# Kernel optimization log

Hardware: AMD Instinct MI355X
Metric: run time of the kernel (lower is better)

The kernel has to match this reference:

```python
import jax, jax.numpy as jnp
import numpy as np

EPS = 1e-5
SCALE = 0.25
H = 16  # num_heads

def _bn(x, gamma, beta):
    # training-mode BatchNorm1d over (batch, length) per channel; x: [M, C, N]
    mean = jnp.mean(x, axis=(0, 2), keepdims=True)
    var = jnp.var(x, axis=(0, 2), keepdims=True)
    return gamma[None, :, None] * (x - mean) * jax.lax.rsqrt(var + EPS) + beta[None, :, None]

def _spike(x, vth):
    # fresh MyNode within one forward: mem = 0/tau + x, spike if >= vth
    return (x >= vth).astype(x.dtype)

def setup_inputs() -> dict:
    key = jax.random.key(0)
    ks = jax.random.split(key, 8)
    T, B, C, N = 4, 1, 256, 1024
    x = jax.random.normal(ks[0], (T, B, C, N), dtype=jnp.float32)
    y = jax.random.normal(ks[1], (T, B, C, N), dtype=jnp.float32)
    def w(k):
        return jax.random.normal(k, (C, C), dtype=jnp.float32) * (1.0 / np.sqrt(C))
    return {
        "x": x, "y": y,
        "Wq": w(ks[2]), "gq": jnp.ones((C,), jnp.float32), "bq": jnp.zeros((C,), jnp.float32),
        "Wk": w(ks[3]), "gk": jnp.ones((C,), jnp.float32), "bk": jnp.zeros((C,), jnp.float32),
        "Wv": w(ks[4]), "gv": jnp.ones((C,), jnp.float32), "bv": jnp.zeros((C,), jnp.float32),
        "Wp": w(ks[5]), "gp": jnp.ones((C,), jnp.float32), "bp": jnp.zeros((C,), jnp.float32),
    }

def reference(x, y, Wq, gq, bq, Wk, gk, bk, Wv, gv, bv, Wp, gp, bp):
    T, B, C, N = x.shape
    D = C // H
    xf = x.reshape(T * B, C, N)
    yf = y.reshape(T * B, C, N)

    def branch(inp, W, g, b, vth):
        h = jnp.einsum('oc,mcn->mon', W, inp)      # conv1x1
        h = _bn(h, g, b)
        s = _spike(h, vth)                          # LIF spike (fresh state)
        # [T,B,C,N] -> split channels into heads -> [T,B,H,N,D]
        return s.reshape(T, B, H, D, N).transpose(0, 1, 2, 4, 3)

    q = branch(xf, Wq, gq, bq, 1.0)
    k = branch(yf, Wk, gk, bk, 1.0)
    v = branch(yf, Wv, gv, bv, 1.0)

    attn = jnp.einsum('tbhnd,tbhmd->tbhnm', q, k)   # [T,B,H,N,N]
    out = jnp.einsum('tbhnm,tbhmd->tbhnd', attn, v) * SCALE

    # [T,B,H,N,D] -> [T,B,C,N]
    out = out.transpose(0, 1, 2, 4, 3).reshape(T, B, C, N)
    out = _spike(out.reshape(T * B, C, N), 0.5)      # attn_lif, v_threshold=0.5
    out = jnp.einsum('oc,mcn->mon', Wp, out)         # proj conv1x1
    out = _spike(_bn(out, gp, bp), 1.0)              # proj_bn + proj_lif
    return out.reshape(T, B, C, N)
```

## Files before the change

kernel.cpp:

```cpp
#include <hip/hip_runtime.h>
#include <cstdint>
#include <cstddef>

static constexpr int C = 256;
static constexpr int N = 1024;
static constexpr int M = 4;
static constexpr size_t PLANE = (size_t)M * C * N;

typedef double d4 __attribute__((ext_vector_type(4)));

__device__ inline void probe_d_layout(int lane, int rowv[4], int colv[4])
{
    const double am = (lane < 16) ? (double)lane : 0.0;
    const double a1 = (lane < 16) ? 1.0 : 0.0;
    const double bn = (lane < 16) ? (double)(lane & 15) : 0.0;
    d4 z = (d4){0.0, 0.0, 0.0, 0.0};
    d4 dr = __builtin_amdgcn_mfma_f64_16x16x4f64(am, a1, z, 0, 0, 0);
    d4 dc = __builtin_amdgcn_mfma_f64_16x16x4f64(a1, bn, z, 0, 0, 0);
    #pragma unroll
    for (int r = 0; r < 4; ++r) {
        rowv[r] = (int)dr[r];
        colv[r] = (int)dc[r];
    }
}

static constexpr int ASTR = 36;
static constexpr int BSTR = 72;

__global__ __launch_bounds__(256) void gemm_qkv_mfma(
    const float* __restrict__ x, const float* __restrict__ y,
    const float* __restrict__ Wq, const float* __restrict__ Wk,
    const float* __restrict__ Wv, double* __restrict__ hbase)
{
    const int bz = blockIdx.z;
    const int br = bz >> 2;
    const int m  = bz & 3;
    const float* __restrict__ W = (br == 0) ? Wq : (br == 1) ? Wk : Wv;
    const float* __restrict__ X = ((br == 0) ? x : y) + (size_t)m * C * N;
    double* __restrict__ H = hbase + (size_t)br * PLANE + (size_t)m * C * N;

    const int n0 = blockIdx.x * 64;
    const int o0 = blockIdx.y * 64;
    const int tid  = threadIdx.x;
    const int lane = tid & 63;
    const int w    = tid >> 6;
    const int ow   = (w & 1) * 32;
    const int nw   = (w >> 1) * 32;
    const int lm   = lane & 15;
    const int lk   = lane >> 4;

    int rowv[4], colv[4];
    probe_d_layout(lane, rowv, colv);

    __shared__ __align__(16) float As[2][64 * ASTR];
    __shared__ __align__(16) float Bs[2][32 * BSTR];

    d4 acc[2][2];
    #pragma unroll
    for (int i = 0; i < 2; ++i)
        #pragma unroll
        for (int j = 0; j < 2; ++j)
            acc[i][j] = (d4){0.0, 0.0, 0.0, 0.0};

    const int rA = tid >> 2;
    const int cA = (tid & 3) * 8;
    const int rB = tid >> 3;
    const int cB = (tid & 7) * 8;

    float4 a0r, a1r, b0r, b1r;
    a0r = *(const float4*)(W + (size_t)(o0 + rA) * C + 0 + cA);
    a1r = *(const float4*)(W + (size_t)(o0 + rA) * C + 0 + cA + 4);
    b0r = *(const float4*)(X + (size_t)(0 + rB) * N + n0 + cB);
    b1r = *(const float4*)(X + (size_t)(0 + rB) * N + n0 + cB + 4);

    int buf = 0;
    for (int ch = 0; ch < 8; ++ch) {
        *(float4*)(&As[buf][rA * ASTR + cA])     = a0r;
        *(float4*)(&As[buf][rA * ASTR + cA + 4]) = a1r;
        *(float4*)(&Bs[buf][rB * BSTR + cB])     = b0r;
        *(float4*)(&Bs[buf][rB * BSTR + cB + 4]) = b1r;
        __syncthreads();
        if (ch < 7) {
            const int c0 = (ch + 1) * 32;
            a0r = *(const float4*)(W + (size_t)(o0 + rA) * C + c0 + cA);
            a1r = *(const float4*)(W + (size_t)(o0 + rA) * C + c0 + cA + 4);
            b0r = *(const float4*)(X + (size_t)(c0 + rB) * N + n0 + cB);
            b1r = *(const float4*)(X + (size_t)(c0 + rB) * N + n0 + cB + 4);
        }
        const float* __restrict__ Ab = As[buf];
        const float* __restrict__ Bb = Bs[buf];
        #pragma unroll
        for (int ks = 0; ks < 8; ++ks) {
            const int kk = ks * 4 + lk;
            double a0 = (double)Ab[(ow + lm) * ASTR + kk];
            double a1 = (double)Ab[(ow + 16 + lm) * ASTR + kk];
            double b0 = (double)Bb[kk * BSTR + nw + lm];
            double b1 = (double)Bb[kk * BSTR + nw + 16 + lm];
            acc[0][0] = __builtin_amdgcn_mfma_f64_16x16x4f64(a0, b0, acc[0][0], 0, 0, 0);
            acc[0][1] = __builtin_amdgcn_mfma_f64_16x16x4f64(a0, b1, acc[0][1], 0, 0, 0);
            acc[1][0] = __builtin_amdgcn_mfma_f64_16x16x4f64(a1, b0, acc[1][0], 0, 0, 0);
            acc[1][1] = __builtin_amdgcn_mfma_f64_16x16x4f64(a1, b1, acc[1][1], 0, 0, 0);
        }
        buf ^= 1;
    }

    #pragma unroll
    for (int ot = 0; ot < 2; ++ot)
        #pragma unroll
        for (int nt = 0; nt < 2; ++nt)
            #pragma unroll
            for (int r = 0; r < 4; ++r)
                H[(size_t)(o0 + ow + ot * 16 + rowv[r]) * N + (n0 + nw + nt * 16 + colv[r])] =
                    acc[ot][nt][r];
}

__global__ __launch_bounds__(256) void gemm_p_mfma(
    const float* __restrict__ Wp, const unsigned char* __restrict__ s2,
    double* __restrict__ hp)
{
    const int m = blockIdx.z;
    const unsigned char* __restrict__ X = s2 + (size_t)m * C * N;
    double* __restrict__ H = hp + (size_t)m * C * N;

    const int n0 = blockIdx.x * 64;
    const int o0 = blockIdx.y * 32;
    const int tid  = threadIdx.x;
    const int lane = tid & 63;
    const int w    = tid >> 6;
    const int ow   = (w & 1) * 16;
    const int nw   = (w >> 1) * 32;
    const int lm   = lane & 15;
    const int lk   = lane >> 4;

    int rowv[4], colv[4];
    probe_d_layout(lane, rowv, colv);

    __shared__ __align__(16) float As[2][32 * ASTR];
    __shared__ __align__(16) float Bs[2][32 * BSTR];

    d4 acc[2];
    acc[0] = (d4){0.0, 0.0, 0.0, 0.0};
    acc[1] = (d4){0.0, 0.0, 0.0, 0.0};

    const int rA = tid >> 3;
    const int cA = (tid & 7) * 4;
    const int rB = tid >> 3;
    const int cB = (tid & 7) * 8;

    float4 ar;
    uint2 bw;
    ar = *(const float4*)(Wp + (size_t)(o0 + rA) * C + 0 + cA);
    bw = *(const uint2*)(X + (size_t)(0 + rB) * N + n0 + cB);

    int buf = 0;
    for (int ch = 0; ch < 8; ++ch) {
        *(float4*)(&As[buf][rA * ASTR + cA]) = ar;
        float* bs = &Bs[buf][rB * BSTR + cB];
        bs[0] = (float)(bw.x & 0xFF);
        bs[1] = (float)((bw.x >> 8) & 0xFF);
        bs[2] = (float)((bw.x >> 16) & 0xFF);
        bs[3] = (float)((bw.x >> 24) & 0xFF);
        bs[4] = (float)(bw.y & 0xFF);
        bs[5] = (float)((bw.y >> 8) & 0xFF);
        bs[6] = (float)((bw.y >> 16) & 0xFF);
        bs[7] = (float)((bw.y >> 24) & 0xFF);
        __syncthreads();
        if (ch < 7) {
            const int c0 = (ch + 1) * 32;
            ar = *(const float4*)(Wp + (size_t)(o0 + rA) * C + c0 + cA);
            bw = *(const uint2*)(X + (size_t)(c0 + rB) * N + n0 + cB);
        }
        const float* __restrict__ Ab = As[buf];
        const float* __restrict__ Bb = Bs[buf];
        #pragma unroll
        for (int ks = 0; ks < 8; ++ks) {
            const int kk = ks * 4 + lk;
            double a0 = (double)Ab[(ow + lm) * ASTR + kk];
            double b0 = (double)Bb[kk * BSTR + nw + lm];
            double b1 = (double)Bb[kk * BSTR + nw + 16 + lm];
            acc[0] = __builtin_amdgcn_mfma_f64_16x16x4f64(a0, b0, acc[0], 0, 0, 0);
            acc[1] = __builtin_amdgcn_mfma_f64_16x16x4f64(a0, b1, acc[1], 0, 0, 0);
        }
        buf ^= 1;
    }

    #pragma unroll
    for (int nt = 0; nt < 2; ++nt)
        #pragma unroll
        for (int r = 0; r < 4; ++r)
            H[(size_t)(o0 + ow + rowv[r]) * N + (n0 + nw + nt * 16 + colv[r])] =
                acc[nt][r];
}

__global__ __launch_bounds__(256) void bnspike_qkv(
    const double* __restrict__ hbase,
    const float* __restrict__ gq, const float* __restrict__ bq,
    const float* __restrict__ gk, const float* __restrict__ bk,
    const float* __restrict__ gv, const float* __restrict__ bv,
    unsigned char* __restrict__ sbase)
{
    const int o  = blockIdx.x;
    const int br = blockIdx.y;
    const double* __restrict__ h = hbase + (size_t)br * PLANE + (size_t)o * N;
    const int tid = threadIdx.x;

    double2 v[8];
    double s = 0.0, ss = 0.0;
    #pragma unroll
    for (int j = 0; j < 8; ++j) {
        int idx = j * 512 + tid * 2;
        int mm = idx >> 10, nn = idx & 1023;
        v[j] = *(const double2*)(h + (size_t)mm * C * N + nn);
        s  += v[j].x + v[j].y;
        ss += v[j].x * v[j].x + v[j].y * v[j].y;
    }
    #pragma unroll
    for (int off = 32; off > 0; off >>= 1) {
        s  += __shfl_down(s, off, 64);
        ss += __shfl_down(ss, off, 64);
    }
    __shared__ double rs[4], rss[4], sstat[2];
    const int lane = tid & 63, wv_ = tid >> 6;
    if (lane == 0) { rs[wv_] = s; rss[wv_] = ss; }
    __syncthreads();
    if (tid == 0) {
        double S  = rs[0] + rs[1] + rs[2] + rs[3];
        double SS = rss[0] + rss[1] + rss[2] + rss[3];
        double mean = S / 4096.0;
        double var  = SS / 4096.0 - mean * mean;
        sstat[0] = mean;
        sstat[1] = 1.0 / sqrt(var + 1e-5);
    }
    __syncthreads();
    const double mean = sstat[0], inv = sstat[1];
    const float* g = (br == 0) ? gq : (br == 1) ? gk : gv;
    const float* b = (br == 0) ? bq : (br == 1) ? bk : bv;
    const double gc = (double)g[o], bc = (double)b[o];
    unsigned char* out = sbase + (size_t)br * PLANE + (size_t)o * N;
    #pragma unroll
    for (int j = 0; j < 8; ++j) {
        int idx = j * 512 + tid * 2;
        int mm = idx >> 10, nn = idx & 1023;
        double t0 = gc * (v[j].x - mean) * inv + bc;
        double t1 = gc * (v[j].y - mean) * inv + bc;
        unsigned short pk = (unsigned short)((t0 >= 1.0) ? 1u : 0u) |
                            (unsigned short)(((t1 >= 1.0) ? 1u : 0u) << 8);
        *(unsigned short*)(out + (size_t)mm * C * N + nn) = pk;
    }
}

__global__ __launch_bounds__(256) void attn_kernel(
    const unsigned char* __restrict__ qb, const unsigned char* __restrict__ kb,
    const unsigned char* __restrict__ vb, unsigned char* __restrict__ s2)
{
    const int nc = blockIdx.x;
    const int hh = blockIdx.y;
    const int t  = blockIdx.z;
    const int tid = threadIdx.x;

    __shared__ unsigned int kw[16][257];
    __shared__ unsigned int vw[16][257];
    __shared__ int kt[256];

    #pragma unroll
    for (int j = 0; j < 4; ++j) {
        int idx = j * 256 + tid;
        int r = idx >> 6, q4 = idx & 63;
        size_t goff = ((size_t)(t * C + hh * 16 + r)) * N + (size_t)q4 * 16;
        uint4 kk = *(const uint4*)(kb + goff);
        uint4 vv = *(const uint4*)(vb + goff);
        kw[r][q4 * 4 + 0] = kk.x; kw[r][q4 * 4 + 1] = kk.y;
        kw[r][q4 * 4 + 2] = kk.z; kw[r][q4 * 4 + 3] = kk.w;
        vw[r][q4 * 4 + 0] = vv.x; vw[r][q4 * 4 + 1] = vv.y;
        vw[r][q4 * 4 + 2] = vv.z; vw[r][q4 * 4 + 3] = vv.w;
    }
    __syncthreads();

    const int d = tid >> 4, dp = tid & 15;
    int sum = 0;
    #pragma unroll 8
    for (int wd = 0; wd < 256; ++wd)
        sum += __popc(kw[d][wd] & vw[dp][wd]);
    kt[tid] = sum;
    __syncthreads();

    const int n = nc * 256 + tid;
    int sums[16];
    #pragma unroll
    for (int i = 0; i < 16; ++i) sums[i] = 0;
    #pragma unroll
    for (int d2 = 0; d2 < 16; ++d2) {
        int qv = (int)qb[((size_t)(t * C + hh * 16 + d2)) * N + n];
        #pragma unroll
        for (int dp2 = 0; dp2 < 16; ++dp2)
            sums[dp2] += qv * kt[d2 * 16 + dp2];
    }
    #pragma unroll
    for (int dp2 = 0; dp2 < 16; ++dp2)
        s2[((size_t)(t * C + hh * 16 + dp2)) * N + n] = (sums[dp2] >= 2) ? 1 : 0;
}

__global__ __launch_bounds__(256) void bnspike_p(
    const double* __restrict__ hp,
    const float* __restrict__ gp, const float* __restrict__ bp,
    float* __restrict__ outp)
{
    const int o = blockIdx.x;
    const double* __restrict__ h = hp + (size_t)o * N;
    const int tid = threadIdx.x;

    double2 v[8];
    double s = 0.0, ss = 0.0;
    #pragma unroll
    for (int j = 0; j < 8; ++j) {
        int idx = j * 512 + tid * 2;
        int mm = idx >> 10, nn = idx & 1023;
        v[j] = *(const double2*)(h + (size_t)mm * C * N + nn);
        s  += v[j].x + v[j].y;
        ss += v[j].x * v[j].x + v[j].y * v[j].y;
    }
    #pragma unroll
    for (int off = 32; off > 0; off >>= 1) {
        s  += __shfl_down(s, off, 64);
        ss += __shfl_down(ss, off, 64);
    }
    __shared__ double rs[4], rss[4], sstat[2];
    const int lane = tid & 63, wv_ = tid >> 6;
    if (lane == 0) { rs[wv_] = s; rss[wv_] = ss; }
    __syncthreads();
    if (tid == 0) {
        double S  = rs[0] + rs[1] + rs[2] + rs[3];
        double SS = rss[0] + rss[1] + rss[2] + rss[3];
        double mean = S / 4096.0;
        double var  = SS / 4096.0 - mean * mean;
        sstat[0] = mean;
        sstat[1] = 1.0 / sqrt(var + 1e-5);
    }
    __syncthreads();
    const double mean = sstat[0], inv = sstat[1];
    const double gc = (double)gp[o], bc = (double)bp[o];
    float* out = outp + (size_t)o * N;
    #pragma unroll
    for (int j = 0; j < 8; ++j) {
        int idx = j * 512 + tid * 2;
        int mm = idx >> 10, nn = idx & 1023;
        float2 r;
        r.x = (gc * (v[j].x - mean) * inv + bc >= 1.0) ? 1.0f : 0.0f;
        r.y = (gc * (v[j].y - mean) * inv + bc >= 1.0) ? 1.0f : 0.0f;
        *(float2*)(out + (size_t)mm * C * N + nn) = r;
    }
}

extern "C" void kernel_launch(void* const* d_in, const int* in_sizes, int n_in,
                              void* d_out, int out_size, void* d_ws, size_t ws_size,
                              hipStream_t stream)
{
    const float* x  = (const float*)d_in[0];
    const float* y  = (const float*)d_in[1];
    const float* Wq = (const float*)d_in[2];
    const float* gq = (const float*)d_in[3];
    const float* bq = (const float*)d_in[4];
    const float* Wk = (const float*)d_in[5];
    const float* gk = (const float*)d_in[6];
    const float* bk = (const float*)d_in[7];
    const float* Wv = (const float*)d_in[8];
    const float* gv = (const float*)d_in[9];
    const float* bv = (const float*)d_in[10];
    const float* Wp = (const float*)d_in[11];
    const float* gp = (const float*)d_in[12];
    const float* bp = (const float*)d_in[13];
    float* out = (float*)d_out;

    char* ws = (char*)d_ws;
    double* hq = (double*)ws;
    double* hp = hq;
    unsigned char* qb  = (unsigned char*)(ws + 3 * PLANE * sizeof(double));
    unsigned char* kb2 = qb + PLANE;
    unsigned char* vb2 = qb + 2 * PLANE;
    unsigned char* s2b = qb + 3 * PLANE;

    gemm_qkv_mfma<<<dim3(16, 4, 12), 256, 0, stream>>>(x, y, Wq, Wk, Wv, hq);
    bnspike_qkv<<<dim3(256, 3), 256, 0, stream>>>(hq, gq, bq, gk, bk, gv, bv, qb);
    attn_kernel<<<dim3(4, 16, 4), 256, 0, stream>>>(qb, kb2, vb2, s2b);
    gemm_p_mfma<<<dim3(16, 8, 4), 256, 0, stream>>>(Wp, s2b, hp);
    bnspike_p<<<dim3(256), 256, 0, stream>>>(hp, gp, bp, out);
}
```

Baseline: 148.5 us.

## Replace FP64 MFMA GEMMs with three-way split FP16 MFMA emulation

```diff
diff --git a/kernel.cpp b/kernel.cpp
--- a/kernel.cpp
+++ b/kernel.cpp
@@ -1,229 +1,239 @@
 #include <hip/hip_runtime.h>
 #include <cstdint>
 #include <cstddef>
+#include <cmath>
 
 static constexpr int C = 256;
 static constexpr int N = 1024;
 static constexpr int M = 4;
 static constexpr size_t PLANE = (size_t)M * C * N;
 
-typedef double d4 __attribute__((ext_vector_type(4)));
-
-__device__ inline void probe_d_layout(int lane, int rowv[4], int colv[4])
-{
-    const double am = (lane < 16) ? (double)lane : 0.0;
-    const double a1 = (lane < 16) ? 1.0 : 0.0;
-    const double bn = (lane < 16) ? (double)(lane & 15) : 0.0;
-    d4 z = (d4){0.0, 0.0, 0.0, 0.0};
-    d4 dr = __builtin_amdgcn_mfma_f64_16x16x4f64(am, a1, z, 0, 0, 0);
-    d4 dc = __builtin_amdgcn_mfma_f64_16x16x4f64(a1, bn, z, 0, 0, 0);
-    #pragma unroll
-    for (int r = 0; r < 4; ++r) {
-        rowv[r] = (int)dr[r];
-        colv[r] = (int)dc[r];
-    }
-}
-
-static constexpr int ASTR = 36;
-static constexpr int BSTR = 72;
-
-__global__ __launch_bounds__(256) void gemm_qkv_mfma(
+typedef unsigned short u16;
+typedef u16      u16x8 __attribute__((ext_vector_type(8)));
+typedef u16      u16x4 __attribute__((ext_vector_type(4)));
+typedef _Float16 f16x8 __attribute__((ext_vector_type(8)));
+typedef float    f32x4 __attribute__((ext_vector_type(4)));
+
+static constexpr int FSTR = 40;
+static constexpr size_t LVX = (size_t)8 * 1024 * 256;
+static constexpr size_t LVW = (size_t)4 * 256 * 256;
+
+__device__ __forceinline__ void split3(float v, u16 &h0, u16 &h1, u16 &h2)
+{
+    union { _Float16 f; u16 u; } cv;
+    float a0 = (fabsf(v) >= 6.103515625e-05f) ? v : 0.0f;
+    cv.f = (_Float16)a0;                 h0 = cv.u;
+    float f0 = (float)cv.f;
+    float r1 = v - f0;
+    cv.f = (_Float16)(r1 * 4096.0f);     h1 = cv.u;
+    float f1 = (float)cv.f * 2.44140625e-4f;
+    float r2 = r1 - f1;
+    cv.f = (_Float16)(r2 * 16777216.0f); h2 = cv.u;
+}
+
+__device__ __forceinline__ void probe16(int lane, int rowv[4], int colv[4])
+{
+    f16x8 ar, one, bn;
+    #pragma unroll
+    for (int i = 0; i < 8; ++i){ ar[i]=(_Float16)0.f; one[i]=(_Float16)0.f; bn[i]=(_Float16)0.f; }
+    if (lane < 16){
+        ar[0]  = (_Float16)(float)lane;
+        one[0] = (_Float16)1.0f;
+        bn[0]  = (_Float16)(float)lane;
+    }
+    f32x4 z = (f32x4){0.f,0.f,0.f,0.f};
+    f32x4 dr = __builtin_amdgcn_mfma_f32_16x16x32_f16(ar,  one, z, 0, 0, 0);
+    f32x4 dc = __builtin_amdgcn_mfma_f32_16x16x32_f16(one, bn,  z, 0, 0, 0);
+    #pragma unroll
+    for (int r = 0; r < 4; ++r){ rowv[r] = (int)dr[r]; colv[r] = (int)dc[r]; }
+}
+
+__global__ __launch_bounds__(256) void split_pre(
     const float* __restrict__ x, const float* __restrict__ y,
     const float* __restrict__ Wq, const float* __restrict__ Wk,
-    const float* __restrict__ Wv, double* __restrict__ hbase)
-{
-    const int bz = blockIdx.z;
-    const int br = bz >> 2;
-    const int m  = bz & 3;
-    const float* __restrict__ W = (br == 0) ? Wq : (br == 1) ? Wk : Wv;
-    const float* __restrict__ X = ((br == 0) ? x : y) + (size_t)m * C * N;
-    double* __restrict__ H = hbase + (size_t)br * PLANE + (size_t)m * C * N;
-
-    const int n0 = blockIdx.x * 64;
-    const int o0 = blockIdx.y * 64;
-    const int tid  = threadIdx.x;
-    const int lane = tid & 63;
-    const int w    = tid >> 6;
-    const int ow   = (w & 1) * 32;
-    const int nw   = (w >> 1) * 32;
-    const int lm   = lane & 15;
-    const int lk   = lane >> 4;
+    const float* __restrict__ Wv, const float* __restrict__ Wp,
+    u16* __restrict__ xyT, u16* __restrict__ wsp)
+{
+    const int z = blockIdx.z, tid = threadIdx.x;
+    if (z < 8){
+        const float* __restrict__ src = (z < 4) ? (x + (size_t)z * C * N)
+                                                : (y + (size_t)(z - 4) * C * N);
+        const int n0 = blockIdx.x * 64, c0 = blockIdx.y * 64;
+        __shared__ float Ls[64][65];
+        const int cr = tid >> 2, q = tid & 3;
+        #pragma unroll
+        for (int j = 0; j < 4; ++j){
+            float4 vv = *(const float4*)(src + (size_t)(c0 + cr) * N + n0 + q * 16 + j * 4);
+            *(float4*)&Ls[cr][q * 16 + j * 4] = vv;
+        }
+        __syncthreads();
+        const int nr = tid >> 2, cq = tid & 3;
+        u16 h0[16], h1[16], h2[16];
+        #pragma unroll
+        for (int e = 0; e < 16; ++e)
+            split3(Ls[cq * 16 + e][nr], h0[e], h1[e], h2[e]);
+        const size_t base = (size_t)z * (1024 * 256) + (size_t)(n0 + nr) * C + c0 + cq * 16;
+        u16x8 t0, t1;
+        #pragma unroll
+        for (int i = 0; i < 8; ++i){ t0[i] = h0[i]; t1[i] = h0[8 + i]; }
+        *(u16x8*)(xyT + base) = t0;            *(u16x8*)(xyT + base + 8) = t1;
+        #pragma unroll
+        for (int i = 0; i < 8; ++i){ t0[i] = h1[i]; t1[i] = h1[8 + i]; }
+        *(u16x8*)(xyT + LVX + base) = t0;      *(u16x8*)(xyT + LVX + base + 8) = t1;
+        #pragma unroll
+        for (int i = 0; i < 8; ++i){ t0[i] = h2[i]; t1[i] = h2[8 + i]; }
+        *(u16x8*)(xyT + 2 * LVX + base) = t0;  *(u16x8*)(xyT + 2 * LVX + base + 8) = t1;
+    } else {
+        const float* __restrict__ Wm = (z == 8) ? Wq : (z == 9) ? Wk : (z == 10) ? Wv : Wp;
+        const int idx = ((blockIdx.y * 16 + blockIdx.x) * 256 + tid) * 4;
+        float4 vv = *(const float4*)(Wm + idx);
+        const size_t base = (size_t)(z - 8) * 65536 + idx;
+        u16x4 o0_, o1_, o2_;
+        u16 a, b, c2;
+        split3(vv.x, a, b, c2); o0_[0]=a; o1_[0]=b; o2_[0]=c2;
+        split3(vv.y, a, b, c2); o0_[1]=a; o1_[1]=b; o2_[1]=c2;
+        split3(vv.z, a, b, c2); o0_[2]=a; o1_[2]=b; o2_[2]=c2;
+        split3(vv.w, a, b, c2); o0_[3]=a; o1_[3]=b; o2_[3]=c2;
+        *(u16x4*)(wsp + base) = o0_;
+        *(u16x4*)(wsp + LVW + base) = o1_;
+        *(u16x4*)(wsp + 2 * LVW + base) = o2_;
+    }
+}
+
+__global__ __launch_bounds__(256, 2) void gemm_qkv_f16(
+    const u16* __restrict__ xyT, const u16* __restrict__ wsp,
+    float* __restrict__ hbase)
+{
+    const int bz = blockIdx.z, br = bz >> 2, m = bz & 3;
+    const int plane = (br == 0) ? m : 4 + m;
+    const u16* __restrict__ Xl = xyT + (size_t)plane * 1024 * 256;
+    const u16* __restrict__ Wl = wsp + (size_t)br * 65536;
+    float* __restrict__ H = hbase + (size_t)br * PLANE + (size_t)m * C * N;
+
+    const int n0 = blockIdx.x * 64, o0 = blockIdx.y * 64;
+    const int tid = threadIdx.x, lane = tid & 63, w = tid >> 6;
+    const int ow = (w & 1) * 32, nw = (w >> 1) * 32, lm = lane & 15, lk = lane >> 4;
 
     int rowv[4], colv[4];
-    probe_d_layout(lane, rowv, colv);
-
-    __shared__ __align__(16) float As[2][64 * ASTR];
-    __shared__ __align__(16) float Bs[2][32 * BSTR];
-
-    d4 acc[2][2];
+    probe16(lane, rowv, colv);
+
+    __shared__ __align__(16) u16 As[2][3][64 * FSTR];
+    __shared__ __align__(16) u16 Bs[2][3][64 * FSTR];
+
+    f32x4 ah[2][2], am2[2][2], al[2][2];
+    double hs[2][2][4];
     #pragma unroll
     for (int i = 0; i < 2; ++i)
         #pragma unroll
-        for (int j = 0; j < 2; ++j)
-            acc[i][j] = (d4){0.0, 0.0, 0.0, 0.0};
-
-    const int rA = tid >> 2;
-    const int cA = (tid & 3) * 8;
-    const int rB = tid >> 3;
-    const int cB = (tid & 7) * 8;
-
-    float4 a0r, a1r, b0r, b1r;
-    a0r = *(const float4*)(W + (size_t)(o0 + rA) * C + 0 + cA);
-    a1r = *(const float4*)(W + (size_t)(o0 + rA) * C + 0 + cA + 4);
-    b0r = *(const float4*)(X + (size_t)(0 + rB) * N + n0 + cB);
-    b1r = *(const float4*)(X + (size_t)(0 + rB) * N + n0 + cB + 4);
+        for (int j = 0; j < 2; ++j){
+            ah[i][j] = (f32x4){0.f,0.f,0.f,0.f};
+            am2[i][j] = (f32x4){0.f,0.f,0.f,0.f};
+            al[i][j] = (f32x4){0.f,0.f,0.f,0.f};
+            #pragma unroll
+            for (int r = 0; r < 4; ++r) hs[i][j][r] = 0.0;
+        }
+
+    const int rA = tid >> 2, c8 = (tid & 3) * 8;
+    u16x8 aR[3], bR[3];
+    #pragma unroll
+    for (int lv = 0; lv < 3; ++lv){
+        aR[lv] = *(const u16x8*)(Wl + (size_t)lv * LVW + (size_t)(o0 + rA) * C + c8);
+        bR[lv] = *(const u16x8*)(Xl + (size_t)lv * LVX + (size_t)(n0 + rA) * C + c8);
+    }
 
     int buf = 0;
-    for (int ch = 0; ch < 8; ++ch) {
-        *(float4*)(&As[buf][rA * ASTR + cA])     = a0r;
-        *(float4*)(&As[buf][rA * ASTR + cA + 4]) = a1r;
-        *(float4*)(&Bs[buf][rB * BSTR + cB])     = b0r;
-        *(float4*)(&Bs[buf][rB * BSTR + cB + 4]) = b1r;
+    for (int ch = 0; ch < 8; ++ch){
+        #pragma unroll
+        for (int lv = 0; lv < 3; ++lv){
+            *(u16x8*)&As[buf][lv][rA * FSTR + c8] = aR[lv];
+            *(u16x8*)&Bs[buf][lv][rA * FSTR + c8] = bR[lv];
+        }
         __syncthreads();
-        if (ch < 7) {
-            const int c0 = (ch + 1) * 32;
-            a0r = *(const float4*)(W + (size_t)(o0 + rA) * C + c0 + cA);
-            a1r = *(const float4*)(W + (size_t)(o0 + rA) * C + c0 + cA + 4);
-            b0r = *(const float4*)(X + (size_t)(c0 + rB) * N + n0 + cB);
-            b1r = *(const float4*)(X + (size_t)(c0 + rB) * N + n0 + cB + 4);
-        }
-        const float* __restrict__ Ab = As[buf];
-        const float* __restrict__ Bb = Bs[buf];
-        #pragma unroll
-        for (int ks = 0; ks < 8; ++ks) {
-            const int kk = ks * 4 + lk;
-            double a0 = (double)Ab[(ow + lm) * ASTR + kk];
-            double a1 = (double)Ab[(ow + 16 + lm) * ASTR + kk];
-            double b0 = (double)Bb[kk * BSTR + nw + lm];
-            double b1 = (double)Bb[kk * BSTR + nw + 16 + lm];
-            acc[0][0] = __builtin_amdgcn_mfma_f64_16x16x4f64(a0, b0, acc[0][0], 0, 0, 0);
-            acc[0][1] = __builtin_amdgcn_mfma_f64_16x16x4f64(a0, b1, acc[0][1], 0, 0, 0);
-            acc[1][0] = __builtin_amdgcn_mfma_f64_16x16x4f64(a1, b0, acc[1][0], 0, 0, 0);
-            acc[1][1] = __builtin_amdgcn_mfma_f64_16x16x4f64(a1, b1, acc[1][1], 0, 0, 0);
+        if (ch < 7){
+            const int cc = (ch + 1) * 32;
+            #pragma unroll
+            for (int lv = 0; lv < 3; ++lv){
+                aR[lv] = *(const u16x8*)(Wl + (size_t)lv * LVW + (size_t)(o0 + rA) * C + cc + c8);
+                bR[lv] = *(const u16x8*)(Xl + (size_t)lv * LVX + (size_t)(n0 + rA) * C + cc + c8);
+            }
+        }
+        f16x8 af[2][3], bf[2][3];
+        #pragma unroll
+        for (int ot = 0; ot < 2; ++ot)
+            #pragma unroll
+            for (int lv = 0; lv < 3; ++lv)
+                af[ot][lv] = *(const f16x8*)&As[buf][lv][(ow + ot * 16 + lm) * FSTR + lk * 8];
+        #pragma unroll
+        for (int nt = 0; nt < 2; ++nt)
+            #pragma unroll
+            for (int lv = 0; lv < 3; ++lv)
+                bf[nt][lv] = *(const f16x8*)&Bs[buf][lv][(nw + nt * 16 + lm) * FSTR + lk * 8];
+        #pragma unroll
+        for (int ot = 0; ot < 2; ++ot)
+            #pragma unroll
+            for (int nt = 0; nt < 2; ++nt){
+                ah[ot][nt]  = __builtin_amdgcn_mfma_f32_16x16x32_f16(af[ot][0], bf[nt][0], ah[ot][nt], 0, 0, 0);
+                am2[ot][nt] = __builtin_amdgcn_mfma_f32_16x16x32_f16(af[ot][0], bf[nt][1], am2[ot][nt], 0, 0, 0);
+                am2[ot][nt] = __builtin_amdgcn_mfma_f32_16x16x32_f16(af[ot][1], bf[nt][0], am2[ot][nt], 0, 0, 0);
+                al[ot][nt]  = __builtin_amdgcn_mfma_f32_16x16x32_f16(af[ot][1], bf[nt][1], al[ot][nt], 0, 0, 0);
+                al[ot][nt]  = __builtin_amdgcn_mfma_f32_16x16x32_f16(af[ot][0], bf[nt][2], al[ot][nt], 0, 0, 0);
+                al[ot][nt]  = __builtin_amdgcn_mfma_f32_16x16x32_f16(af[ot][2], bf[nt][0], al[ot][nt], 0, 0, 0);
+            }
+        if (ch & 1){
+            #pragma unroll
+            for (int ot = 0; ot < 2; ++ot)
+                #pragma unroll
+                for (int nt = 0; nt < 2; ++nt){
+                    #pragma unroll
+                    for (int r = 0; r < 4; ++r) hs[ot][nt][r] += (double)ah[ot][nt][r];
+                    ah[ot][nt] = (f32x4){0.f,0.f,0.f,0.f};
+                }
         }
         buf ^= 1;
     }
 
+    const double S12 = 1.0 / 4096.0, S24 = 1.0 / 16777216.0;
     #pragma unroll
     for (int ot = 0; ot < 2; ++ot)
         #pragma unroll
         for (int nt = 0; nt < 2; ++nt)
             #pragma unroll
-            for (int r = 0; r < 4; ++r)
-                H[(size_t)(o0 + ow + ot * 16 + rowv[r]) * N + (n0 + nw + nt * 16 + colv[r])] =
-                    acc[ot][nt][r];
-}
-
-__global__ __launch_bounds__(256) void gemm_p_mfma(
-    const float* __restrict__ Wp, const unsigned char* __restrict__ s2,
-    double* __restrict__ hp)
-{
-    const int m = blockIdx.z;
-    const unsigned char* __restrict__ X = s2 + (size_t)m * C * N;
-    double* __restrict__ H = hp + (size_t)m * C * N;
-
-    const int n0 = blockIdx.x * 64;
-    const int o0 = blockIdx.y * 32;
-    const int tid  = threadIdx.x;
-    const int lane = tid & 63;
-    const int w    = tid >> 6;
-    const int ow   = (w & 1) * 16;
-    const int nw   = (w >> 1) * 32;
-    const int lm   = lane & 15;
-    const int lk   = lane >> 4;
-
-    int rowv[4], colv[4];
-    probe_d_layout(lane, rowv, colv);
-
-    __shared__ __align__(16) float As[2][32 * ASTR];
-    __shared__ __align__(16) float Bs[2][32 * BSTR];
-
-    d4 acc[2];
-    acc[0] = (d4){0.0, 0.0, 0.0, 0.0};
-    acc[1] = (d4){0.0, 0.0, 0.0, 0.0};
-
-    const int rA = tid >> 3;
-    const int cA = (tid & 7) * 4;
-    const int rB = tid >> 3;
-    const int cB = (tid & 7) * 8;
-
-    float4 ar;
-    uint2 bw;
-    ar = *(const float4*)(Wp + (size_t)(o0 + rA) * C + 0 + cA);
-    bw = *(const uint2*)(X + (size_t)(0 + rB) * N + n0 + cB);
-
-    int buf = 0;
-    for (int ch = 0; ch < 8; ++ch) {
-        *(float4*)(&As[buf][rA * ASTR + cA]) = ar;
-        float* bs = &Bs[buf][rB * BSTR + cB];
-        bs[0] = (float)(bw.x & 0xFF);
-        bs[1] = (float)((bw.x >> 8) & 0xFF);
-        bs[2] = (float)((bw.x >> 16) & 0xFF);
-        bs[3] = (float)((bw.x >> 24) & 0xFF);
-        bs[4] = (float)(bw.y & 0xFF);
-        bs[5] = (float)((bw.y >> 8) & 0xFF);
-        bs[6] = (float)((bw.y >> 16) & 0xFF);
-        bs[7] = (float)((bw.y >> 24) & 0xFF);
-        __syncthreads();
-        if (ch < 7) {
-            const int c0 = (ch + 1) * 32;
-            ar = *(const float4*)(Wp + (size_t)(o0 + rA) * C + c0 + cA);
-            bw = *(const uint2*)(X + (size_t)(c0 + rB) * N + n0 + cB);
-        }
-        const float* __restrict__ Ab = As[buf];
-        const float* __restrict__ Bb = Bs[buf];
-        #pragma unroll
-        for (int ks = 0; ks < 8; ++ks) {
-            const int kk = ks * 4 + lk;
-            double a0 = (double)Ab[(ow + lm) * ASTR + kk];
-            double b0 = (double)Bb[kk * BSTR + nw + lm];
-            double b1 = (double)Bb[kk * BSTR + nw + 16 + lm];
-            acc[0] = __builtin_amdgcn_mfma_f64_16x16x4f64(a0, b0, acc[0], 0, 0, 0);
-            acc[1] = __builtin_amdgcn_mfma_f64_16x16x4f64(a0, b1, acc[1], 0, 0, 0);
-        }
-        buf ^= 1;
-    }
-
-    #pragma unroll
-    for (int nt = 0; nt < 2; ++nt)
-        #pragma unroll
-        for (int r = 0; r < 4; ++r)
-            H[(size_t)(o0 + ow + rowv[r]) * N + (n0 + nw + nt * 16 + colv[r])] =
-                acc[nt][r];
+            for (int r = 0; r < 4; ++r){
+                double hv = hs[ot][nt][r] + (double)am2[ot][nt][r] * S12 + (double)al[ot][nt][r] * S24;
+                H[(size_t)(o0 + ow + ot * 16 + rowv[r]) * N + (n0 + nw + nt * 16 + colv[r])] = (float)hv;
+            }
 }
 
 __global__ __launch_bounds__(256) void bnspike_qkv(
-    const double* __restrict__ hbase,
+    const float* __restrict__ hbase,
     const float* __restrict__ gq, const float* __restrict__ bq,
     const float* __restrict__ gk, const float* __restrict__ bk,
     const float* __restrict__ gv, const float* __restrict__ bv,
     unsigned char* __restrict__ sbase)
 {
-    const int o  = blockIdx.x;
-    const int br = blockIdx.y;
-    const double* __restrict__ h = hbase + (size_t)br * PLANE + (size_t)o * N;
+    const int o = blockIdx.x, br = blockIdx.y;
+    const float* __restrict__ h = hbase + (size_t)br * PLANE + (size_t)o * N;
     const int tid = threadIdx.x;
 
-    double2 v[8];
+    float4 v[4];
     double s = 0.0, ss = 0.0;
     #pragma unroll
-    for (int j = 0; j < 8; ++j) {
-        int idx = j * 512 + tid * 2;
-        int mm = idx >> 10, nn = idx & 1023;
-        v[j] = *(const double2*)(h + (size_t)mm * C * N + nn);
-        s  += v[j].x + v[j].y;
-        ss += v[j].x * v[j].x + v[j].y * v[j].y;
-    }
-    #pragma unroll
-    for (int off = 32; off > 0; off >>= 1) {
+    for (int j = 0; j < 4; ++j){
+        v[j] = *(const float4*)(h + (size_t)j * C * N + tid * 4);
+        double a = v[j].x, b = v[j].y, c = v[j].z, d = v[j].w;
+        s  += (a + b) + (c + d);
+        ss += (a * a + b * b) + (c * c + d * d);
+    }
+    #pragma unroll
+    for (int off = 32; off > 0; off >>= 1){
         s  += __shfl_down(s, off, 64);
         ss += __shfl_down(ss, off, 64);
     }
     __shared__ double rs[4], rss[4], sstat[2];
     const int lane = tid & 63, wv_ = tid >> 6;
-    if (lane == 0) { rs[wv_] = s; rss[wv_] = ss; }
-    __syncthreads();
-    if (tid == 0) {
+    if (lane == 0){ rs[wv_] = s; rss[wv_] = ss; }
+    __syncthreads();
+    if (tid == 0){
         double S  = rs[0] + rs[1] + rs[2] + rs[3];
         double SS = rss[0] + rss[1] + rss[2] + rss[3];
         double mean = S / 4096.0;
@@ -238,20 +248,19 @@
     const double gc = (double)g[o], bc = (double)b[o];
     unsigned char* out = sbase + (size_t)br * PLANE + (size_t)o * N;
     #pragma unroll
-    for (int j = 0; j < 8; ++j) {
-        int idx = j * 512 + tid * 2;
-        int mm = idx >> 10, nn = idx & 1023;
-        double t0 = gc * (v[j].x - mean) * inv + bc;
-        double t1 = gc * (v[j].y - mean) * inv + bc;
-        unsigned short pk = (unsigned short)((t0 >= 1.0) ? 1u : 0u) |
-                            (unsigned short)(((t1 >= 1.0) ? 1u : 0u) << 8);
-        *(unsigned short*)(out + (size_t)mm * C * N + nn) = pk;
+    for (int j = 0; j < 4; ++j){
+        unsigned int pk = 0;
+        pk |= ((gc * ((double)v[j].x - mean) * inv + bc >= 1.0) ? 1u : 0u);
+        pk |= ((gc * ((double)v[j].y - mean) * inv + bc >= 1.0) ? 1u : 0u) << 8;
+        pk |= ((gc * ((double)v[j].z - mean) * inv + bc >= 1.0) ? 1u : 0u) << 16;
+        pk |= ((gc * ((double)v[j].w - mean) * inv + bc >= 1.0) ? 1u : 0u) << 24;
+        *(unsigned int*)(out + (size_t)j * C * N + tid * 4) = pk;
     }
 }
 
 __global__ __launch_bounds__(256) void attn_kernel(
     const unsigned char* __restrict__ qb, const unsigned char* __restrict__ kb,
-    const unsigned char* __restrict__ vb, unsigned char* __restrict__ s2)
+    const unsigned char* __restrict__ vb, unsigned char* __restrict__ s2T)
 {
     const int nc = blockIdx.x;
     const int hh = blockIdx.y;
@@ -263,7 +272,7 @@
     __shared__ int kt[256];
 
     #pragma unroll
-    for (int j = 0; j < 4; ++j) {
+    for (int j = 0; j < 4; ++j){
         int idx = j * 256 + tid;
         int r = idx >> 6, q4 = idx & 63;
         size_t goff = ((size_t)(t * C + hh * 16 + r)) * N + (size_t)q4 * 16;
@@ -289,46 +298,145 @@
     #pragma unroll
     for (int i = 0; i < 16; ++i) sums[i] = 0;
     #pragma unroll
-    for (int d2 = 0; d2 < 16; ++d2) {
+    for (int d2 = 0; d2 < 16; ++d2){
         int qv = (int)qb[((size_t)(t * C + hh * 16 + d2)) * N + n];
         #pragma unroll
         for (int dp2 = 0; dp2 < 16; ++dp2)
             sums[dp2] += qv * kt[d2 * 16 + dp2];
     }
-    #pragma unroll
-    for (int dp2 = 0; dp2 < 16; ++dp2)
-        s2[((size_t)(t * C + hh * 16 + dp2)) * N + n] = (sums[dp2] >= 2) ? 1 : 0;
+    uint4 ov;
+    unsigned int* ovp = (unsigned int*)&ov;
+    #pragma unroll
+    for (int g = 0; g < 4; ++g){
+        unsigned int wv2 = 0;
+        #pragma unroll
+        for (int e = 0; e < 4; ++e)
+            wv2 |= ((sums[g * 4 + e] >= 2) ? 1u : 0u) << (8 * e);
+        ovp[g] = wv2;
+    }
+    *(uint4*)(s2T + ((size_t)t * N + n) * C + hh * 16) = ov;
+}
+
+__global__ __launch_bounds__(256, 2) void gemm_p_f16(
+    const u16* __restrict__ wsp, const unsigned char* __restrict__ s2T,
+    float* __restrict__ hp)
+{
+    const int m = blockIdx.z;
+    const int n0 = blockIdx.x * 64, o0 = blockIdx.y * 32;
+    const int tid = threadIdx.x, lane = tid & 63, w = tid >> 6;
+    const int ow = (w & 1) * 16, nw = (w >> 1) * 32, lm = lane & 15, lk = lane >> 4;
+    const u16* __restrict__ Wl = wsp + (size_t)3 * 65536;
+    const unsigned char* __restrict__ Xb = s2T + (size_t)m * N * C;
+    float* __restrict__ H = hp + (size_t)m * C * N;
+
+    int rowv[4], colv[4];
+    probe16(lane, rowv, colv);
+
+    __shared__ __align__(16) u16 As[2][3][32 * FSTR];
+    __shared__ __align__(16) u16 Bs[2][64 * FSTR];
+
+    f32x4 a0[2], a1[2], a2[2];
+    double hs[2][4];
+    #pragma unroll
+    for (int i = 0; i < 2; ++i){
+        a0[i] = (f32x4){0.f,0.f,0.f,0.f};
+        a1[i] = (f32x4){0.f,0.f,0.f,0.f};
+        a2[i] = (f32x4){0.f,0.f,0.f,0.f};
+        #pragma unroll
+        for (int r = 0; r < 4; ++r) hs[i][r] = 0.0;
+    }
+
+    const int rA = tid >> 3, c4 = (tid & 7) * 4;
+    const int rB = tid >> 2, c8 = (tid & 3) * 8;
+    u16x4 aR[3];
+    uint2 bw;
+    #pragma unroll
+    for (int lv = 0; lv < 3; ++lv)
+        aR[lv] = *(const u16x4*)(Wl + (size_t)lv * LVW + (size_t)(o0 + rA) * C + c4);
+    bw = *(const uint2*)(Xb + (size_t)(n0 + rB) * C + c8);
+
+    int buf = 0;
+    for (int ch = 0; ch < 8; ++ch){
+        #pragma unroll
+        for (int lv = 0; lv < 3; ++lv)
+            *(u16x4*)&As[buf][lv][rA * FSTR + c4] = aR[lv];
+        u16x8 bv;
+        #pragma unroll
+        for (int e = 0; e < 4; ++e){
+            bv[e]     = (u16)(((bw.x >> (8 * e)) & 1u) * 0x3C00u);
+            bv[4 + e] = (u16)(((bw.y >> (8 * e)) & 1u) * 0x3C00u);
+        }
+        *(u16x8*)&Bs[buf][rB * FSTR + c8] = bv;
+        __syncthreads();
+        if (ch < 7){
+            const int cc = (ch + 1) * 32;
+            #pragma unroll
+            for (int lv = 0; lv < 3; ++lv)
+                aR[lv] = *(const u16x4*)(Wl + (size_t)lv * LVW + (size_t)(o0 + rA) * C + cc + c4);
+            bw = *(const uint2*)(Xb + (size_t)(n0 + rB) * C + cc + c8);
+        }
+        f16x8 af[3], bf[2];
+        #pragma unroll
+        for (int lv = 0; lv < 3; ++lv)
+            af[lv] = *(const f16x8*)&As[buf][lv][(ow + lm) * FSTR + lk * 8];
+        #pragma unroll
+        for (int nt = 0; nt < 2; ++nt)
+            bf[nt] = *(const f16x8*)&Bs[buf][(nw + nt * 16 + lm) * FSTR + lk * 8];
+        #pragma unroll
+        for (int nt = 0; nt < 2; ++nt){
+            a0[nt] = __builtin_amdgcn_mfma_f32_16x16x32_f16(af[0], bf[nt], a0[nt], 0, 0, 0);
+            a1[nt] = __builtin_amdgcn_mfma_f32_16x16x32_f16(af[1], bf[nt], a1[nt], 0, 0, 0);
+            a2[nt] = __builtin_amdgcn_mfma_f32_16x16x32_f16(af[2], bf[nt], a2[nt], 0, 0, 0);
+        }
+        if (ch & 1){
+            #pragma unroll
+            for (int nt = 0; nt < 2; ++nt){
+                #pragma unroll
+                for (int r = 0; r < 4; ++r) hs[nt][r] += (double)a0[nt][r];
+                a0[nt] = (f32x4){0.f,0.f,0.f,0.f};
+            }
+        }
+        buf ^= 1;
+    }
+
+    const double S12 = 1.0 / 4096.0, S24 = 1.0 / 16777216.0;
+    #pragma unroll
+    for (int nt = 0; nt < 2; ++nt)
+        #pragma unroll
+        for (int r = 0; r < 4; ++r){
+            double hv = hs[nt][r] + (double)a1[nt][r] * S12 + (double)a2[nt][r] * S24;
+            H[(size_t)(o0 + ow + rowv[r]) * N + (n0 + nw + nt * 16 + colv[r])] = (float)hv;
+        }
 }
 
 __global__ __launch_bounds__(256) void bnspike_p(
-    const double* __restrict__ hp,
+    const float* __restrict__ hp,
     const float* __restrict__ gp, const float* __restrict__ bp,
     float* __restrict__ outp)
 {
     const int o = blockIdx.x;
-    const double* __restrict__ h = hp + (size_t)o * N;
+    const float* __restrict__ h = hp + (size_t)o * N;
     const int tid = threadIdx.x;
 
-    double2 v[8];
+    float4 v[4];
     double s = 0.0, ss = 0.0;
     #pragma unroll
-    for (int j = 0; j < 8; ++j) {
-        int idx = j * 512 + tid * 2;
-        int mm = idx >> 10, nn = idx & 1023;
-        v[j] = *(const double2*)(h + (size_t)mm * C * N + nn);
-        s  += v[j].x + v[j].y;
-        ss += v[j].x * v[j].x + v[j].y * v[j].y;
-    }
-    #pragma unroll
-    for (int off = 32; off > 0; off >>= 1) {
+    for (int j = 0; j < 4; ++j){
+        v[j] = *(const float4*)(h + (size_t)j * C * N + tid * 4);
+        double a = v[j].x, b = v[j].y, c = v[j].z, d = v[j].w;
+        s  += (a + b) + (c + d);
+        ss += (a * a + b * b) + (c * c + d * d);
+    }
+    #pragma unroll
+    for (int off = 32; off > 0; off >>= 1){
         s  += __shfl_down(s, off, 64);
         ss += __shfl_down(ss, off, 64);
     }
     __shared__ double rs[4], rss[4], sstat[2];
     const int lane = tid & 63, wv_ = tid >> 6;
-    if (lane == 0) { rs[wv_] = s; rss[wv_] = ss; }
-    __syncthreads();
-    if (tid == 0) {
+    if (lane == 0){ rs[wv_] = s; rss[wv_] = ss; }
+    __syncthreads();
+    if (tid == 0){
         double S  = rs[0] + rs[1] + rs[2] + rs[3];
         double SS = rss[0] + rss[1] + rss[2] + rss[3];
         double mean = S / 4096.0;
@@ -341,13 +449,13 @@
     const double gc = (double)gp[o], bc = (double)bp[o];
     float* out = outp + (size_t)o * N;
     #pragma unroll
-    for (int j = 0; j < 8; ++j) {
-        int idx = j * 512 + tid * 2;
-        int mm = idx >> 10, nn = idx & 1023;
-        float2 r;
-        r.x = (gc * (v[j].x - mean) * inv + bc >= 1.0) ? 1.0f : 0.0f;
-        r.y = (gc * (v[j].y - mean) * inv + bc >= 1.0) ? 1.0f : 0.0f;
-        *(float2*)(out + (size_t)mm * C * N + nn) = r;
+    for (int j = 0; j < 4; ++j){
+        float4 r;
+        r.x = (gc * ((double)v[j].x - mean) * inv + bc >= 1.0) ? 1.0f : 0.0f;
+        r.y = (gc * ((double)v[j].y - mean) * inv + bc >= 1.0) ? 1.0f : 0.0f;
+        r.z = (gc * ((double)v[j].z - mean) * inv + bc >= 1.0) ? 1.0f : 0.0f;
+        r.w = (gc * ((double)v[j].w - mean) * inv + bc >= 1.0) ? 1.0f : 0.0f;
+        *(float4*)(out + (size_t)j * C * N + tid * 4) = r;
     }
 }
 
@@ -372,16 +480,19 @@
     float* out = (float*)d_out;
 
     char* ws = (char*)d_ws;
-    double* hq = (double*)ws;
-    double* hp = hq;
-    unsigned char* qb  = (unsigned char*)(ws + 3 * PLANE * sizeof(double));
+    u16* xyT = (u16*)ws;
+    u16* wsp = (u16*)(ws + (size_t)12 * 1024 * 1024);
+    float* hq = (float*)(ws + (size_t)14 * 1024 * 1024);
+    float* hp = hq;
+    unsigned char* qb  = (unsigned char*)ws;
     unsigned char* kb2 = qb + PLANE;
     unsigned char* vb2 = qb + 2 * PLANE;
     unsigned char* s2b = qb + 3 * PLANE;
 
-    gemm_qkv_mfma<<<dim3(16, 4, 12), 256, 0, stream>>>(x, y, Wq, Wk, Wv, hq);
+    split_pre<<<dim3(16, 4, 12), 256, 0, stream>>>(x, y, Wq, Wk, Wv, Wp, xyT, wsp);
+    gemm_qkv_f16<<<dim3(16, 4, 12), 256, 0, stream>>>(xyT, wsp, hq);
     bnspike_qkv<<<dim3(256, 3), 256, 0, stream>>>(hq, gq, bq, gk, bk, gv, bv, qb);
     attn_kernel<<<dim3(4, 16, 4), 256, 0, stream>>>(qb, kb2, vb2, s2b);
-    gemm_p_mfma<<<dim3(16, 8, 4), 256, 0, stream>>>(Wp, s2b, hp);
+    gemm_p_f16<<<dim3(16, 8, 4), 256, 0, stream>>>(wsp, s2b, hp);
     bnspike_p<<<dim3(256), 256, 0, stream>>>(hp, gp, bp, out);
 }
```

Result: faster. 127.7 us (-14.0%).
